# Kernel optimization log

Hardware: AMD Instinct MI355X
Metric: run time of the kernel (lower is better)

The kernel has to match this reference:

```python
import jax, jax.numpy as jnp
import numpy as np

NEG_SLOPE = 0.2

def gat_conv(x, src, dst, W, a_src, a_dst, bias, N):
    # PyG GATConv, heads=1: h = xW; e_ij = LeakyReLU(a_src.h_j + a_dst.h_i)
    h = x @ W                                   # [N, H]
    as_ = h @ a_src                             # [N]
    ad_ = h @ a_dst                             # [N]
    e = jax.nn.leaky_relu(as_[src] + ad_[dst], NEG_SLOPE)   # [E]
    m = jax.ops.segment_max(e, dst, num_segments=N)          # per-target max
    w = jnp.exp(e - m[dst])
    denom = jax.ops.segment_sum(w, dst, num_segments=N)
    alpha = w / (denom[dst] + 1e-16)                          # [E]
    out = jax.ops.segment_sum(alpha[:, None] * h[src], dst, num_segments=N)
    return out + bias


def setup_inputs() -> dict:
    key = jax.random.key(0)
    N, E, D, H, A = 20000, 320000, 256, 256, 8
    ks = jax.random.split(key, 16)
    s = lambda k, shp, fan: jax.random.normal(k, shp, jnp.float32) * (1.0 / np.sqrt(fan))
    return {
        "obs": jax.random.normal(ks[0], (N, D), jnp.float32),
        "edge_index": jax.random.randint(ks[1], (2, E), 0, N, dtype=jnp.int32),
        "W1": s(ks[2], (D, H), D), "a1_src": s(ks[3], (H,), H), "a1_dst": s(ks[4], (H,), H), "b1": jnp.zeros((H,), jnp.float32),
        "W2": s(ks[5], (H, H), H), "a2_src": s(ks[6], (H,), H), "a2_dst": s(ks[7], (H,), H), "b2": jnp.zeros((H,), jnp.float32),
        "Wm1": s(ks[8], (H, H), H), "bm1": jnp.zeros((H,), jnp.float32),
        "Wm2": s(ks[9], (H, A), H), "bm2": jnp.zeros((A,), jnp.float32),
    }


def reference(obs, edge_index, W1, a1_src, a1_dst, b1, W2, a2_src, a2_dst, b2, Wm1, bm1, Wm2, bm2):
    N = obs.shape[0]
    loops = jnp.arange(N, dtype=edge_index.dtype)
    src = jnp.concatenate([edge_index[0], loops])   # add self-loops (PyG default)
    dst = jnp.concatenate([edge_index[1], loops])
    x = jax.nn.relu(gat_conv(obs, src, dst, W1, a1_src, a1_dst, b1, N))
    x = jax.nn.relu(gat_conv(x,   src, dst, W2, a2_src, a2_dst, b2, N))
    x = jax.nn.relu(x @ Wm1 + bm1)
    return jnp.tanh(x @ Wm2 + bm2)
```

## Files before the change

### kernel.cpp

```cpp
#include <hip/hip_runtime.h>
#include <hip/hip_bf16.h>
#include <math.h>

typedef __attribute__((ext_vector_type(8))) short short8;
typedef __attribute__((ext_vector_type(4))) float f32x4;
typedef __attribute__((ext_vector_type(8))) unsigned short us8;

__device__ __forceinline__ float us2f(unsigned short u) {
    return __uint_as_float(((unsigned)u) << 16);
}
__device__ __forceinline__ unsigned short f2us_rtn(float f) {
    return (unsigned short)__bfloat16_as_ushort(__float2bfloat16(f));
}

__global__ void prep_all(const float* __restrict__ Wa, const float* __restrict__ Wb,
                         const float* __restrict__ Wc, const float* __restrict__ obs,
                         unsigned short* __restrict__ TA, unsigned short* __restrict__ TB,
                         unsigned short* __restrict__ TC, unsigned short* __restrict__ obsb,
                         float* __restrict__ as1, float* __restrict__ ad1,
                         float* __restrict__ as2, float* __restrict__ ad2,
                         int* __restrict__ deg,
                         int K, int Nn, int N, int nObs8) {
    const int tot = K * Nn;
    int idx = blockIdx.x * blockDim.x + threadIdx.x;
    if (idx < 3 * tot) {
        const float* W;
        unsigned short* T;
        if (idx < tot) { W = Wa; T = TA; }
        else if (idx < 2 * tot) { W = Wb; T = TB; idx -= tot; }
        else { W = Wc; T = TC; idx -= 2 * tot; }
        const int n = idx / K, k = idx - n * K;
        T[idx] = f2us_rtn(W[(size_t)k * Nn + n]);
        return;
    }
    idx -= 3 * tot;
    if (idx < 5 * N) {
        if (idx < N) as1[idx] = 0.f;
        else if (idx < 2 * N) ad1[idx - N] = 0.f;
        else if (idx < 3 * N) as2[idx - 2 * N] = 0.f;
        else if (idx < 4 * N) ad2[idx - 3 * N] = 0.f;
        else deg[idx - 4 * N] = 0;
        return;
    }
    idx -= 5 * N;
    if (idx < nObs8) {
        const float4 a = *(const float4*)(obs + (size_t)idx * 8);
        const float4 b = *(const float4*)(obs + (size_t)idx * 8 + 4);
        const float f[8] = {a.x, a.y, a.z, a.w, b.x, b.y, b.z, b.w};
        short8 o;
#pragma unroll
        for (int e = 0; e < 8; e++) o[e] = (short)f2us_rtn(f[e]);
        *(short8*)(obsb + (size_t)idx * 8) = o;
    }
}

#define LPB 264
__global__ __launch_bounds__(256, 4) void gemm_mfma(const unsigned short* __restrict__ A,
                                                    const unsigned short* __restrict__ Bt,
                                                    const float* __restrict__ avs,
                                                    const float* __restrict__ avd,
                                                    float* __restrict__ as_,
                                                    float* __restrict__ ad_,
                                                    unsigned short* __restrict__ C,
                                                    int M, int Nn, int K) {
    __shared__ unsigned short sB[64 * LPB];
    const int tid = threadIdx.x;
    const int wave = tid >> 6, lane = tid & 63;
    const int m16 = lane & 15, quad = lane >> 4;
    const int row0 = blockIdx.x * 64, col0 = blockIdx.y * 64;
    const int wr = wave * 16;

    {
        const int c = tid >> 2, kc0 = (tid & 3) * 64;
        const unsigned short* Bp = Bt + (size_t)(col0 + c) * K + kc0;
        unsigned short* dp = &sB[c * LPB + kc0];
#pragma unroll
        for (int j = 0; j < 8; j++)
            *(short8*)(dp + j * 8) = *(const short8*)(Bp + j * 8);
    }

    int gr = row0 + wr + m16;
    if (gr >= M) gr = M - 1;
    const unsigned short* Arow = A + (size_t)gr * K + quad * 8;
    short8 a0 = *(const short8*)(Arow);
    short8 a1 = *(const short8*)(Arow + 32);
    short8 a2 = *(const short8*)(Arow + 64);
    short8 a3 = *(const short8*)(Arow + 96);
    __syncthreads();

    f32x4 acc[4] = {};
    const unsigned short* sBl = &sB[m16 * LPB + quad * 8];
#define BSTEP(af, kk)                                                              \
    {                                                                              \
        _Pragma("unroll")                                                          \
        for (int ni = 0; ni < 4; ni++) {                                           \
            const short8 bv = *(const short8*)(sBl + ni * (16 * LPB) + (kk));      \
            acc[ni] = __builtin_amdgcn_mfma_f32_16x16x32_bf16(af, bv, acc[ni], 0, 0, 0); \
        }                                                                          \
    }
    for (int k0 = 0; k0 < K; k0 += 128) {
        const bool more = (k0 + 128) < K;
        short8 n0, n1, n2, n3;
        if (more) {
            n0 = *(const short8*)(Arow + k0 + 128);
            n1 = *(const short8*)(Arow + k0 + 160);
            n2 = *(const short8*)(Arow + k0 + 192);
            n3 = *(const short8*)(Arow + k0 + 224);
        }
        BSTEP(a0, k0)
        BSTEP(a1, k0 + 32)
        BSTEP(a2, k0 + 64)
        BSTEP(a3, k0 + 96)
        if (!more) break;
        a0 = n0; a1 = n1; a2 = n2; a3 = n3;
    }
#undef BSTEP

    float ps[4] = {}, pd[4] = {};
    const int orow_base = row0 + wr + quad * 4;
#pragma unroll
    for (int ni = 0; ni < 4; ni++) {
        const int ocol = col0 + ni * 16 + m16;
        const float asv = avs[ocol], adv = avd[ocol];
#pragma unroll
        for (int r = 0; r < 4; r++) {
            const int orow = orow_base + r;
            if (orow < M) {
                const float v = acc[ni][r];
                C[(size_t)orow * Nn + ocol] = f2us_rtn(v);
                ps[r] = fmaf(v, asv, ps[r]);
                pd[r] = fmaf(v, adv, pd[r]);
            }
        }
    }
#pragma unroll
    for (int r = 0; r < 4; r++)
#pragma unroll
        for (int off = 1; off < 16; off <<= 1) {
            ps[r] += __shfl_xor(ps[r], off);
            pd[r] += __shfl_xor(pd[r], off);
        }
    if (m16 == 0) {
#pragma unroll
        for (int r = 0; r < 4; r++) {
            const int orow = orow_base + r;
            if (orow < M) {
                atomicAdd(&as_[orow], ps[r]);
                atomicAdd(&ad_[orow], pd[r]);
            }
        }
    }
}
#undef LPB

#define LP 72
__global__ __launch_bounds__(256) void gemm_head(const unsigned short* __restrict__ A,
                                                 const unsigned short* __restrict__ Bt,
                                                 const float* __restrict__ bias1,
                                                 const float* __restrict__ W2,
                                                 const float* __restrict__ bias2,
                                                 float* __restrict__ out,
                                                 int M, int K, int Aout) {
    __shared__ unsigned short sA[64 * LP];
    __shared__ unsigned short sB[256 * LP];
    __shared__ float pLDS[2][64][8];
    const int tid = threadIdx.x;
    const int wave = tid >> 6, lane = tid & 63;
    const int m16 = lane & 15, quad = lane >> 4;
    const int row0 = blockIdx.x * 64;
    const int wr = (wave >> 1) * 32, wc = (wave & 1) * 128;
    const int ar = tid >> 2, akc = (tid & 3) * 8;
    const int bkc = (tid & 7) * 8, bcb = tid >> 3;
    const int gr = (row0 + ar) < M ? (row0 + ar) : (M - 1);
    const unsigned short* Arow = A + (size_t)gr * K + akc;
    const unsigned short* Bcol = Bt + (size_t)bcb * K + bkc;

    short8 rA0, rA1, rb[8];
    auto LOADT = [&](int k0) {
        rA0 = *(const short8*)(Arow + k0);
        rA1 = *(const short8*)(Arow + k0 + 32);
#pragma unroll
        for (int q = 0; q < 8; q++)
            rb[q] = *(const short8*)(Bcol + (size_t)(32 * q) * K + k0);
    };
    auto STORET = [&]() {
        *(short8*)&sA[ar * LP + akc]      = rA0;
        *(short8*)&sA[ar * LP + akc + 32] = rA1;
#pragma unroll
        for (int q = 0; q < 8; q++)
            *(short8*)&sB[(bcb + 32 * q) * LP + bkc] = rb[q];
    };

    f32x4 acc[2][8] = {};
    LOADT(0);
    STORET();
    __syncthreads();
    for (int k0 = 0; k0 < K; k0 += 64) {
        const bool more = (k0 + 64) < K;
        if (more) LOADT(k0 + 64);
#pragma unroll
        for (int ks = 0; ks < 2; ks++) {
            short8 ah[2];
#pragma unroll
            for (int mi = 0; mi < 2; mi++)
                ah[mi] = *(const short8*)&sA[(wr + mi * 16 + m16) * LP + ks * 32 + quad * 8];
#pragma unroll
            for (int ni = 0; ni < 8; ni++) {
                const short8 bv = *(const short8*)&sB[(wc + ni * 16 + m16) * LP + ks * 32 + quad * 8];
#pragma unroll
                for (int mi = 0; mi < 2; mi++)
                    acc[mi][ni] = __builtin_amdgcn_mfma_f32_16x16x32_bf16(ah[mi], bv, acc[mi][ni], 0, 0, 0);
            }
        }
        __syncthreads();
        if (more) { STORET(); __syncthreads(); }
    }
    float p[2][4][8] = {};
#pragma unroll
    for (int ni = 0; ni < 8; ni++) {
        const int ocol = wc + ni * 16 + m16;
        const float b1v = bias1[ocol];
        float w2[8];
#pragma unroll
        for (int a = 0; a < 8; a++) w2[a] = W2[ocol * 8 + a];
#pragma unroll
        for (int mi = 0; mi < 2; mi++)
#pragma unroll
            for (int r = 0; r < 4; r++) {
                const float v = fmaxf(acc[mi][ni][r] + b1v, 0.f);
#pragma unroll
                for (int a = 0; a < 8; a++) p[mi][r][a] = fmaf(v, w2[a], p[mi][r][a]);
            }
    }
#pragma unroll
    for (int off = 1; off < 16; off <<= 1)
#pragma unroll
        for (int mi = 0; mi < 2; mi++)
#pragma unroll
            for (int r = 0; r < 4; r++)
#pragma unroll
                for (int a = 0; a < 8; a++) p[mi][r][a] += __shfl_xor(p[mi][r][a], off);
    if (m16 == 0) {
        const int half = wc >> 7;
#pragma unroll
        for (int mi = 0; mi < 2; mi++) {
            const int lrow = wr + mi * 16 + quad * 4;
#pragma unroll
            for (int r = 0; r < 4; r++)
#pragma unroll
                for (int a = 0; a < 8; a++) pLDS[half][lrow + r][a] = p[mi][r][a];
        }
    }
    __syncthreads();
#pragma unroll
    for (int u = 0; u < 2; u++) {
        const int idx = tid * 2 + u;
        const int lrow = idx >> 3, a = idx & 7;
        const int orow = row0 + lrow;
        if (orow < M && a < Aout)
            out[(size_t)orow * Aout + a] =
                tanhf(pLDS[0][lrow][a] + pLDS[1][lrow][a] + bias2[a]);
    }
}
#undef LP

__global__ void count_kernel(const int* __restrict__ dstA, int* __restrict__ deg, int E, int Etot) {
    const int e = blockIdx.x * blockDim.x + threadIdx.x;
    if (e >= Etot) return;
    const int d = (e < E) ? dstA[e] : (e - E);
    atomicAdd(&deg[d], 1);
}

__global__ __launch_bounds__(1024) void scan_kernel(const int* __restrict__ deg,
                                                    int* __restrict__ offs,
                                                    int* __restrict__ cursor, int N) {
    __shared__ int sums[1024];
    const int t = threadIdx.x;
    const int chunk = (N + 1023) / 1024;
    const int start = t * chunk;
    int s = 0;
    for (int i = 0; i < chunk; i++) {
        const int p = start + i;
        if (p < N) s += deg[p];
    }
    sums[t] = s;
    __syncthreads();
    for (int off = 1; off < 1024; off <<= 1) {
        const int add = (t >= off) ? sums[t - off] : 0;
        __syncthreads();
        sums[t] += add;
        __syncthreads();
    }
    int run = (t > 0) ? sums[t - 1] : 0;
    for (int i = 0; i < chunk; i++) {
        const int p = start + i;
        if (p < N) { offs[p] = run; cursor[p] = run; run += deg[p]; }
    }
    if (t == 0) offs[N] = sums[1023];
}

__global__ void scatter_kernel(const int* __restrict__ srcA, const int* __restrict__ dstA,
                               int* __restrict__ cursor, int* __restrict__ esrc, int E, int Etot) {
    const int e = blockIdx.x * blockDim.x + threadIdx.x;
    if (e >= Etot) return;
    int s, d;
    if (e < E) { s = srcA[e]; d = dstA[e]; } else { s = d = e - E; }
    const int slot = atomicAdd(&cursor[d], 1);
    esrc[slot] = s;
}

__global__ __launch_bounds__(256) void agg_kernel(const unsigned short* __restrict__ hb,
                                                  const int* __restrict__ offs,
                                                  const int* __restrict__ esrc,
                                                  const float* __restrict__ as_,
                                                  const float* __restrict__ ad_,
                                                  const float* __restrict__ bias,
                                                  unsigned short* __restrict__ xout, int N) {
    const int n = __builtin_amdgcn_readfirstlane(blockIdx.x * 4 + (threadIdx.x >> 6));
    if (n >= N) return;
    const int lane = threadIdx.x & 63;
    const int half = lane >> 5;
    const int f0 = (lane & 31) * 8;
    const int b = offs[n], e2 = offs[n + 1];
    const float adn = ad_[n];
    float a[8] = {};
    float wsum = 0.f;
    for (int c0 = b; c0 < e2; c0 += 16) {
        int s = 0;
        float w = 0.f;
        if (lane < 16) {
            const int j = c0 + lane;
            const int jj = j < e2 ? j : e2 - 1;
            s = esrc[jj];
            if (j < e2) {
                float v = as_[s] + adn;
                v = v > 0.f ? v : 0.2f * v;
                w = __expf(v);
                wsum += w;
            }
        }
        us8 pv[8];
        float wb[8];
#pragma unroll
        for (int u = 0; u < 8; u++) {
            const int el = 2 * u + half;
            const int su = __shfl(s, el);
            wb[u] = __shfl(w, el);
            pv[u] = *(const us8*)(hb + (unsigned)((su << 8) + f0));
        }
#pragma unroll
        for (int u = 0; u < 8; u++)
#pragma unroll
            for (int j2 = 0; j2 < 8; j2++)
                a[j2] = fmaf(wb[u], us2f(pv[u][j2]), a[j2]);
    }
#pragma unroll
    for (int j2 = 0; j2 < 8; j2++) a[j2] += __shfl_xor(a[j2], 32);
#pragma unroll
    for (int off = 32; off; off >>= 1) wsum += __shfl_xor(wsum, off);
    const float inv = 1.0f / (wsum + 1e-16f);
    if (half == 0) {
        const float4 b0 = *(const float4*)(bias + f0);
        const float4 b1 = *(const float4*)(bias + f0 + 4);
        const float bb[8] = {b0.x, b0.y, b0.z, b0.w, b1.x, b1.y, b1.z, b1.w};
        us8 o;
#pragma unroll
        for (int j2 = 0; j2 < 8; j2++)
            o[j2] = f2us_rtn(fmaxf(a[j2] * inv + bb[j2], 0.f));
        *(us8*)(xout + (unsigned)((n << 8) + f0)) = o;
    }
}

extern "C" void kernel_launch(void* const* d_in, const int* in_sizes, int n_in,
                              void* d_out, int out_size, void* d_ws, size_t ws_size,
                              hipStream_t stream) {
    const float* obs = (const float*)d_in[0];
    const int* eidx  = (const int*)d_in[1];
    const float* W1  = (const float*)d_in[2];
    const float* a1s = (const float*)d_in[3];
    const float* a1d = (const float*)d_in[4];
    const float* b1  = (const float*)d_in[5];
    const float* W2  = (const float*)d_in[6];
    const float* a2s = (const float*)d_in[7];
    const float* a2d = (const float*)d_in[8];
    const float* b2v = (const float*)d_in[9];
    const float* Wm1 = (const float*)d_in[10];
    const float* bm1 = (const float*)d_in[11];
    const float* Wm2 = (const float*)d_in[12];
    const float* bm2 = (const float*)d_in[13];
    float* out = (float*)d_out;

    const int Hh = in_sizes[3];
    const int Dd = in_sizes[2] / Hh;
    const int N  = in_sizes[0] / Dd;
    const int E  = in_sizes[1] / 2;
    const int Etot = E + N;
    const int Aout = in_sizes[12] / Hh;

    const int* srcA = eidx;
    const int* dstA = eidx + E;

    size_t off = 0;
    char* ws = (char*)d_ws;
    auto alloc = [&](size_t bytes) -> char* {
        char* p = ws + off;
        off = (off + bytes + 15) & ~(size_t)15;
        return p;
    };
    unsigned short* h    = (unsigned short*)alloc((size_t)N * Hh * 2);
    unsigned short* xb   = (unsigned short*)alloc((size_t)N * Hh * 2);
    unsigned short* obsb = (unsigned short*)alloc((size_t)N * Dd * 2);
    float* as1   = (float*)alloc((size_t)N * 4);
    float* ad1   = (float*)alloc((size_t)N * 4);
    float* as2   = (float*)alloc((size_t)N * 4);
    float* ad2   = (float*)alloc((size_t)N * 4);
    int* deg     = (int*)alloc((size_t)N * 4);
    int* offs    = (int*)alloc((size_t)(N + 1) * 4);
    int* cursor  = (int*)alloc((size_t)N * 4);
    int* esrc    = (int*)alloc((size_t)Etot * 4);
    const size_t wsz = (size_t)Dd * Hh;
    unsigned short* W1t = (unsigned short*)alloc(wsz * 2);
    unsigned short* W2t = (unsigned short*)alloc(wsz * 2);
    unsigned short* Wmt = (unsigned short*)alloc(wsz * 2);

    const int eb = 256;
    const int eg = (Etot + eb - 1) / eb;
    const int nrow = (N + 63) / 64;
    const dim3 ggrid(nrow, Hh / 64);
    const int nb4 = (N + 3) / 4;
    const int nObs8 = N * Dd / 8;

    const int ptot = 3 * (int)wsz + 5 * N + nObs8;
    prep_all<<<(ptot + 255) / 256, 256, 0, stream>>>(
        W1, W2, Wm1, obs, W1t, W2t, Wmt, obsb, as1, ad1, as2, ad2, deg, Dd, Hh, N, nObs8);

    count_kernel<<<eg, eb, 0, stream>>>(dstA, deg, E, Etot);
    scan_kernel<<<1, 1024, 0, stream>>>(deg, offs, cursor, N);
    scatter_kernel<<<eg, eb, 0, stream>>>(srcA, dstA, cursor, esrc, E, Etot);

    gemm_mfma<<<ggrid, 256, 0, stream>>>(obsb, W1t, a1s, a1d, as1, ad1, h, N, Hh, Dd);
    agg_kernel<<<nb4, 256, 0, stream>>>(h, offs, esrc, as1, ad1, b1, xb, N);

    gemm_mfma<<<ggrid, 256, 0, stream>>>(xb, W2t, a2s, a2d, as2, ad2, h, N, Hh, Hh);
    agg_kernel<<<nb4, 256, 0, stream>>>(h, offs, esrc, as2, ad2, b2v, xb, N);

    gemm_head<<<nrow, 256, 0, stream>>>(xb, Wmt, bm1, Wm2, bm2, out, N, Hh, Aout);
}
```

Baseline: 269.5 us.

## Fuse first GEMM, degree count and last-block scan into one kernel

Result: slower. 317.0 us (+17.6%).

```diff
diff --git a/kernel.cpp b/kernel.cpp
--- a/kernel.cpp
+++ b/kernel.cpp
@@ -13,16 +13,17 @@
     return (unsigned short)__bfloat16_as_ushort(__float2bfloat16(f));
 }
 
-__global__ void prep_all(const float* __restrict__ Wa, const float* __restrict__ Wb,
-                         const float* __restrict__ Wc, const float* __restrict__ obs,
-                         unsigned short* __restrict__ TA, unsigned short* __restrict__ TB,
-                         unsigned short* __restrict__ TC, unsigned short* __restrict__ obsb,
-                         float* __restrict__ as1, float* __restrict__ ad1,
-                         float* __restrict__ as2, float* __restrict__ ad2,
-                         int* __restrict__ deg,
-                         int K, int Nn, int N, int nObs8) {
+__global__ void prep_zero(const float* __restrict__ Wa, const float* __restrict__ Wb,
+                          const float* __restrict__ Wc, const float* __restrict__ obs,
+                          unsigned short* __restrict__ TA, unsigned short* __restrict__ TB,
+                          unsigned short* __restrict__ TC, unsigned short* __restrict__ obsb,
+                          float* __restrict__ as1, float* __restrict__ ad1,
+                          float* __restrict__ as2, float* __restrict__ ad2,
+                          int* __restrict__ deg, int* __restrict__ done,
+                          int K, int Nn, int N, int Npad, int nObs8) {
     const int tot = K * Nn;
     int idx = blockIdx.x * blockDim.x + threadIdx.x;
+    if (idx == 0) *done = 0;
     if (idx < 3 * tot) {
         const float* W;
         unsigned short* T;
@@ -34,15 +35,16 @@
         return;
     }
     idx -= 3 * tot;
-    if (idx < 5 * N) {
+    if (idx < 4 * N) {
         if (idx < N) as1[idx] = 0.f;
         else if (idx < 2 * N) ad1[idx - N] = 0.f;
         else if (idx < 3 * N) as2[idx - 2 * N] = 0.f;
-        else if (idx < 4 * N) ad2[idx - 3 * N] = 0.f;
-        else deg[idx - 4 * N] = 0;
+        else ad2[idx - 3 * N] = 0.f;
         return;
     }
-    idx -= 5 * N;
+    idx -= 4 * N;
+    if (idx < Npad) { deg[idx] = 0; return; }
+    idx -= Npad;
     if (idx < nObs8) {
         const float4 a = *(const float4*)(obs + (size_t)idx * 8);
         const float4 b = *(const float4*)(obs + (size_t)idx * 8 + 4);
@@ -55,6 +57,174 @@
 }
 
 #define LPB 264
+__device__ __forceinline__ void gemm_tile64(const unsigned short* __restrict__ A,
+                                            const unsigned short* __restrict__ Bt,
+                                            const float* __restrict__ avs,
+                                            const float* __restrict__ avd,
+                                            float* __restrict__ as_,
+                                            float* __restrict__ ad_,
+                                            unsigned short* __restrict__ C,
+                                            int M, int Nn, int K, int row0, int col0,
+                                            unsigned short* sB) {
+    const int tid = threadIdx.x;
+    const int wave = tid >> 6, lane = tid & 63;
+    const int m16 = lane & 15, quad = lane >> 4;
+    const int wr = wave * 16;
+
+    {
+        const int c = tid >> 2, kc0 = (tid & 3) * 64;
+        const unsigned short* Bp = Bt + (size_t)(col0 + c) * K + kc0;
+        unsigned short* dp = &sB[c * LPB + kc0];
+#pragma unroll
+        for (int j = 0; j < 8; j++)
+            *(short8*)(dp + j * 8) = *(const short8*)(Bp + j * 8);
+    }
+
+    int gr = row0 + wr + m16;
+    if (gr >= M) gr = M - 1;
+    const unsigned short* Arow = A + (size_t)gr * K + quad * 8;
+    short8 a0 = *(const short8*)(Arow);
+    short8 a1 = *(const short8*)(Arow + 32);
+    short8 a2 = *(const short8*)(Arow + 64);
+    short8 a3 = *(const short8*)(Arow + 96);
+    __syncthreads();
+
+    f32x4 acc[4] = {};
+    const unsigned short* sBl = &sB[m16 * LPB + quad * 8];
+#define BSTEP(af, kk)                                                              \
+    {                                                                              \
+        _Pragma("unroll")                                                          \
+        for (int ni = 0; ni < 4; ni++) {                                           \
+            const short8 bv = *(const short8*)(sBl + ni * (16 * LPB) + (kk));      \
+            acc[ni] = __builtin_amdgcn_mfma_f32_16x16x32_bf16(af, bv, acc[ni], 0, 0, 0); \
+        }                                                                          \
+    }
+    for (int k0 = 0; k0 < K; k0 += 128) {
+        const bool more = (k0 + 128) < K;
+        short8 n0, n1, n2, n3;
+        if (more) {
+            n0 = *(const short8*)(Arow + k0 + 128);
+            n1 = *(const short8*)(Arow + k0 + 160);
+            n2 = *(const short8*)(Arow + k0 + 192);
+            n3 = *(const short8*)(Arow + k0 + 224);
+        }
+        BSTEP(a0, k0)
+        BSTEP(a1, k0 + 32)
+        BSTEP(a2, k0 + 64)
+        BSTEP(a3, k0 + 96)
+        if (!more) break;
+        a0 = n0; a1 = n1; a2 = n2; a3 = n3;
+    }
+#undef BSTEP
+
+    float ps[4] = {}, pd[4] = {};
+    const int orow_base = row0 + wr + quad * 4;
+#pragma unroll
+    for (int ni = 0; ni < 4; ni++) {
+        const int ocol = col0 + ni * 16 + m16;
+        const float asv = avs[ocol], adv = avd[ocol];
+#pragma unroll
+        for (int r = 0; r < 4; r++) {
+            const int orow = orow_base + r;
+            if (orow < M) {
+                const float v = acc[ni][r];
+                C[(size_t)orow * Nn + ocol] = f2us_rtn(v);
+                ps[r] = fmaf(v, asv, ps[r]);
+                pd[r] = fmaf(v, adv, pd[r]);
+            }
+        }
+    }
+#pragma unroll
+    for (int r = 0; r < 4; r++)
+#pragma unroll
+        for (int off = 1; off < 16; off <<= 1) {
+            ps[r] += __shfl_xor(ps[r], off);
+            pd[r] += __shfl_xor(pd[r], off);
+        }
+    if (m16 == 0) {
+#pragma unroll
+        for (int r = 0; r < 4; r++) {
+            const int orow = orow_base + r;
+            if (orow < M) {
+                atomicAdd(&as_[orow], ps[r]);
+                atomicAdd(&ad_[orow], pd[r]);
+            }
+        }
+    }
+}
+
+__device__ __forceinline__ void scan_body(const int* __restrict__ deg,
+                                          int* __restrict__ offs,
+                                          int* __restrict__ cursor,
+                                          int N, int per, int* sums) {
+    const int t = threadIdx.x;
+    const int base = t * per;
+    int s = 0;
+    for (int i = 0; i < per; i += 4) {
+        const int4 v = *(const int4*)(deg + base + i);
+        s += v.x + v.y + v.z + v.w;
+    }
+    sums[t] = s;
+    __syncthreads();
+    for (int off = 1; off < 256; off <<= 1) {
+        const int add = (t >= off) ? sums[t - off] : 0;
+        __syncthreads();
+        sums[t] += add;
+        __syncthreads();
+    }
+    int run = (t > 0) ? sums[t - 1] : 0;
+    for (int i = 0; i < per; i += 4) {
+        const int4 v = *(const int4*)(deg + base + i);
+        const int p = base + i;
+        const int vv[4] = {v.x, v.y, v.z, v.w};
+#pragma unroll
+        for (int j = 0; j < 4; j++) {
+            if (p + j < N) { offs[p + j] = run; cursor[p + j] = run; }
+            run += vv[j];
+        }
+    }
+    if (t == 255) offs[N] = run;
+}
+
+__global__ __launch_bounds__(256, 4) void fused_cg(const unsigned short* __restrict__ A,
+                                                   const unsigned short* __restrict__ Bt,
+                                                   const float* __restrict__ avs,
+                                                   const float* __restrict__ avd,
+                                                   float* __restrict__ as_,
+                                                   float* __restrict__ ad_,
+                                                   unsigned short* __restrict__ C,
+                                                   int M, int Nn, int K, int ntiles4,
+                                                   const int* __restrict__ dstA,
+                                                   int* __restrict__ deg, int E, int Etot,
+                                                   int* __restrict__ offs,
+                                                   int* __restrict__ cursor,
+                                                   int* __restrict__ done, int N, int per) {
+    __shared__ unsigned short sB[64 * LPB];
+    __shared__ int sums[256];
+    __shared__ int slast;
+    const int tid = threadIdx.x, bid = blockIdx.x;
+    if (bid < ntiles4) {
+        gemm_tile64(A, Bt, avs, avd, as_, ad_, C, M, Nn, K,
+                    (bid >> 2) * 64, (bid & 3) * 64, sB);
+    } else {
+        const int e = (bid - ntiles4) * 256 + tid;
+        if (e < Etot) {
+            const int d = (e < E) ? dstA[e] : (e - E);
+            atomicAdd(&deg[d], 1);
+        }
+    }
+    __syncthreads();
+    if (tid == 0) {
+        __threadfence();
+        slast = (atomicAdd(done, 1) == (int)gridDim.x - 1);
+    }
+    __syncthreads();
+    if (slast) {
+        __threadfence();
+        scan_body(deg, offs, cursor, N, per, sums);
+    }
+}
+
 __global__ __launch_bounds__(256, 4) void gemm_mfma(const unsigned short* __restrict__ A,
                                                     const unsigned short* __restrict__ Bt,
                                                     const float* __restrict__ avs,
@@ -64,92 +234,8 @@
                                                     unsigned short* __restrict__ C,
                                                     int M, int Nn, int K) {
     __shared__ unsigned short sB[64 * LPB];
-    const int tid = threadIdx.x;
-    const int wave = tid >> 6, lane = tid & 63;
-    const int m16 = lane & 15, quad = lane >> 4;
-    const int row0 = blockIdx.x * 64, col0 = blockIdx.y * 64;
-    const int wr = wave * 16;
-
-    {
-        const int c = tid >> 2, kc0 = (tid & 3) * 64;
-        const unsigned short* Bp = Bt + (size_t)(col0 + c) * K + kc0;
-        unsigned short* dp = &sB[c * LPB + kc0];
-#pragma unroll
-        for (int j = 0; j < 8; j++)
-            *(short8*)(dp + j * 8) = *(const short8*)(Bp + j * 8);
-    }
-
-    int gr = row0 + wr + m16;
-    if (gr >= M) gr = M - 1;
-    const unsigned short* Arow = A + (size_t)gr * K + quad * 8;
-    short8 a0 = *(const short8*)(Arow);
-    short8 a1 = *(const short8*)(Arow + 32);
-    short8 a2 = *(const short8*)(Arow + 64);
-    short8 a3 = *(const short8*)(Arow + 96);
-    __syncthreads();
-
-    f32x4 acc[4] = {};
-    const unsigned short* sBl = &sB[m16 * LPB + quad * 8];
-#define BSTEP(af, kk)                                                              \
-    {                                                                              \
-        _Pragma("unroll")                                                          \
-        for (int ni = 0; ni < 4; ni++) {                                           \
-            const short8 bv = *(const short8*)(sBl + ni * (16 * LPB) + (kk));      \
-            acc[ni] = __builtin_amdgcn_mfma_f32_16x16x32_bf16(af, bv, acc[ni], 0, 0, 0); \
-        }                                                                          \
-    }
-    for (int k0 = 0; k0 < K; k0 += 128) {
-        const bool more = (k0 + 128) < K;
-        short8 n0, n1, n2, n3;
-        if (more) {
-            n0 = *(const short8*)(Arow + k0 + 128);
-            n1 = *(const short8*)(Arow + k0 + 160);
-            n2 = *(const short8*)(Arow + k0 + 192);
-            n3 = *(const short8*)(Arow + k0 + 224);
-        }
-        BSTEP(a0, k0)
-        BSTEP(a1, k0 + 32)
-        BSTEP(a2, k0 + 64)
-        BSTEP(a3, k0 + 96)
-        if (!more) break;
-        a0 = n0; a1 = n1; a2 = n2; a3 = n3;
-    }
-#undef BSTEP
-
-    float ps[4] = {}, pd[4] = {};
-    const int orow_base = row0 + wr + quad * 4;
-#pragma unroll
-    for (int ni = 0; ni < 4; ni++) {
-        const int ocol = col0 + ni * 16 + m16;
-        const float asv = avs[ocol], adv = avd[ocol];
-#pragma unroll
-        for (int r = 0; r < 4; r++) {
-            const int orow = orow_base + r;
-            if (orow < M) {
-                const float v = acc[ni][r];
-                C[(size_t)orow * Nn + ocol] = f2us_rtn(v);
-                ps[r] = fmaf(v, asv, ps[r]);
-                pd[r] = fmaf(v, adv, pd[r]);
-            }
-        }
-    }
-#pragma unroll
-    for (int r = 0; r < 4; r++)
-#pragma unroll
-        for (int off = 1; off < 16; off <<= 1) {
-            ps[r] += __shfl_xor(ps[r], off);
-            pd[r] += __shfl_xor(pd[r], off);
-        }
-    if (m16 == 0) {
-#pragma unroll
-        for (int r = 0; r < 4; r++) {
-            const int orow = orow_base + r;
-            if (orow < M) {
-                atomicAdd(&as_[orow], ps[r]);
-                atomicAdd(&ad_[orow], pd[r]);
-            }
-        }
-    }
+    gemm_tile64(A, Bt, avs, avd, as_, ad_, C, M, Nn, K,
+                blockIdx.x * 64, blockIdx.y * 64, sB);
 }
 #undef LPB
 
@@ -263,41 +349,6 @@
     }
 }
 #undef LP
-
-__global__ void count_kernel(const int* __restrict__ dstA, int* __restrict__ deg, int E, int Etot) {
-    const int e = blockIdx.x * blockDim.x + threadIdx.x;
-    if (e >= Etot) return;
-    const int d = (e < E) ? dstA[e] : (e - E);
-    atomicAdd(&deg[d], 1);
-}
-
-__global__ __launch_bounds__(1024) void scan_kernel(const int* __restrict__ deg,
-                                                    int* __restrict__ offs,
-                                                    int* __restrict__ cursor, int N) {
-    __shared__ int sums[1024];
-    const int t = threadIdx.x;
-    const int chunk = (N + 1023) / 1024;
-    const int start = t * chunk;
-    int s = 0;
-    for (int i = 0; i < chunk; i++) {
-        const int p = start + i;
-        if (p < N) s += deg[p];
-    }
-    sums[t] = s;
-    __syncthreads();
-    for (int off = 1; off < 1024; off <<= 1) {
-        const int add = (t >= off) ? sums[t - off] : 0;
-        __syncthreads();
-        sums[t] += add;
-        __syncthreads();
-    }
-    int run = (t > 0) ? sums[t - 1] : 0;
-    for (int i = 0; i < chunk; i++) {
-        const int p = start + i;
-        if (p < N) { offs[p] = run; cursor[p] = run; run += deg[p]; }
-    }
-    if (t == 0) offs[N] = sums[1023];
-}
 
 __global__ void scatter_kernel(const int* __restrict__ srcA, const int* __restrict__ dstA,
                                int* __restrict__ cursor, int* __restrict__ esrc, int E, int Etot) {
@@ -400,6 +451,10 @@
     const int* srcA = eidx;
     const int* dstA = eidx + E;
 
+    int per = (N + 255) / 256;
+    per = (per + 3) & ~3;
+    const int Npad = 256 * per;
+
     size_t off = 0;
     char* ws = (char*)d_ws;
     auto alloc = [&](size_t bytes) -> char* {
@@ -414,10 +469,11 @@
     float* ad1   = (float*)alloc((size_t)N * 4);
     float* as2   = (float*)alloc((size_t)N * 4);
     float* ad2   = (float*)alloc((size_t)N * 4);
-    int* deg     = (int*)alloc((size_t)N * 4);
+    int* deg     = (int*)alloc((size_t)Npad * 4);
     int* offs    = (int*)alloc((size_t)(N + 1) * 4);
     int* cursor  = (int*)alloc((size_t)N * 4);
     int* esrc    = (int*)alloc((size_t)Etot * 4);
+    int* done    = (int*)alloc(16);
     const size_t wsz = (size_t)Dd * Hh;
     unsigned short* W1t = (unsigned short*)alloc(wsz * 2);
     unsigned short* W2t = (unsigned short*)alloc(wsz * 2);
@@ -426,22 +482,26 @@
     const int eb = 256;
     const int eg = (Etot + eb - 1) / eb;
     const int nrow = (N + 63) / 64;
+    const int ntiles4 = nrow * (Hh / 64);
     const dim3 ggrid(nrow, Hh / 64);
     const int nb4 = (N + 3) / 4;
     const int nObs8 = N * Dd / 8;
 
-    const int ptot = 3 * (int)wsz + 5 * N + nObs8;
-    prep_all<<<(ptot + 255) / 256, 256, 0, stream>>>(
-        W1, W2, Wm1, obs, W1t, W2t, Wmt, obsb, as1, ad1, as2, ad2, deg, Dd, Hh, N, nObs8);
-
-    count_kernel<<<eg, eb, 0, stream>>>(dstA, deg, E, Etot);
-    scan_kernel<<<1, 1024, 0, stream>>>(deg, offs, cursor, N);
+    const int ptot = 3 * (int)wsz + 4 * N + Npad + nObs8;
+    prep_zero<<<(ptot + 255) / 256, 256, 0, stream>>>(
+        W1, W2, Wm1, obs, W1t, W2t, Wmt, obsb, as1, ad1, as2, ad2, deg, done,
+        Dd, Hh, N, Npad, nObs8);
+
+    fused_cg<<<ntiles4 + eg, 256, 0, stream>>>(
+        obsb, W1t, a1s, a1d, as1, ad1, h, N, Hh, Dd, ntiles4,
+        dstA, deg, E, Etot, offs, cursor, done, N, per);
+
     scatter_kernel<<<eg, eb, 0, stream>>>(srcA, dstA, cursor, esrc, E, Etot);
 
-    gemm_mfma<<<ggrid, 256, 0, stream>>>(obsb, W1t, a1s, a1d, as1, ad1, h, N, Hh, Dd);
     agg_kernel<<<nb4, 256, 0, stream>>>(h, offs, esrc, as1, ad1, b1, xb, N);
 
     gemm_mfma<<<ggrid, 256, 0, stream>>>(xb, W2t, a2s, a2d, as2, ad2, h, N, Hh, Hh);
+
     agg_kernel<<<nb4, 256, 0, stream>>>(h, offs, esrc, as2, ad2, b2v, xb, N);
 
     gemm_head<<<nrow, 256, 0, stream>>>(xb, Wmt, bm1, Wm2, bm2, out, N, Hh, Aout);
```
